# Performance work log

Measured on AMD Instinct MI355X. Metric: run time of the kernel, lower is better.

## Reference

```python
import jax, jax.numpy as jnp
import numpy as np

# pywt db4 decomposition low-pass filter (dec_lo), length 8
_DEC_LO = np.array([-0.010597401784997278, 0.032883011666982945,
                    0.030841381835986965, -0.18703481171888114,
                    -0.02798376941698385, 0.6308807679295904,
                    0.7148465705525415, 0.23037781330885523], dtype=np.float32)
FLEN = 8
LEVELS = 9            # pywt.dwt_max_level(4096, 8) == 9
# pywt computes a convolution with dec_lo == correlation with reversed dec_lo
_KERNEL = jnp.asarray(_DEC_LO[::-1].copy()).reshape(1, 1, FLEN)


def _dwt_lo(a):
    """One DWT level (approximation branch only), pywt 'symmetric' mode.
    Output length = floor((n + FLEN - 1) / 2), matching pywt.dwt."""
    pad = [(0, 0)] * (a.ndim - 1) + [(FLEN - 1, FLEN - 1)]
    p = jnp.pad(a, pad, mode='symmetric')[..., 1:]  # correlation starts at offset 1
    bflat = int(np.prod(a.shape[:-1]))
    y = jax.lax.conv_general_dilated(p.reshape(bflat, 1, -1), _KERNEL,
                                     window_strides=(2,), padding='VALID')
    return y.reshape(a.shape[:-1] + (y.shape[-1],))


def wavedec_approx(x):
    a = x
    for _ in range(LEVELS):  # fixed small level count, not a data-dim loop
        a = _dwt_lo(a)
    return a  # [..., 14]


def setup_inputs() -> dict:
    key = jax.random.key(0)
    k1, k2, k3 = jax.random.split(key, 3)
    x = jax.random.normal(k1, (32, 512, 4096), dtype=jnp.float32)
    W = jax.random.normal(k2, (14, 14), dtype=jnp.float32) * (1.0 / np.sqrt(14.0).astype(np.float32))
    b = jax.random.normal(k3, (14,), dtype=jnp.float32) * 0.01
    return {"x": x, "W": W, "b": b}


def reference(x, W, b):
    # original detaches x before the wavelet transform
    approx = wavedec_approx(jax.lax.stop_gradient(x))          # [B, S, 14]
    aug = jnp.einsum('bsf,of->bso', approx, W) + b             # Linear(14, 14)
    return jnp.concatenate([x, aug], axis=-1)                  # [B, S, 4096 + 14]
```

## Files before the change

kernel.cpp:

```cpp
#include <hip/hip_runtime.h>


#define ROWS 16384
#define N0   4096
#define OUTW 4110

__device__ __constant__ float c_dec_lo[8] = {
    -0.010597401784997278f,  0.032883011666982945f,
     0.030841381835986965f, -0.18703481171888114f,
    -0.02798376941698385f,   0.6308807679295904f,
     0.7148465705525415f,    0.23037781330885523f};

__global__ __launch_bounds__(256) void wavelet_aug_kernel(
    const float* __restrict__ x, const float* __restrict__ W,
    const float* __restrict__ b, float* __restrict__ out)
{
    __shared__ float bufA[4096];
    __shared__ float bufB[2051];

    const int row = blockIdx.x;
    const int tid = threadIdx.x;
    const float* xr  = x   + (size_t)row * N0;
    float*       outr = out + (size_t)row * OUTW;

    for (int i = tid; i < N0 / 2; i += 256) {
        float2 v = reinterpret_cast<const float2*>(xr)[i];
        reinterpret_cast<float2*>(outr)[i] = v;
        bufA[2 * i]     = v.x;
        bufA[2 * i + 1] = v.y;
    }
    __syncthreads();

    const int nin_tab[9] = {4096, 2051, 1029, 518, 262, 134, 70, 38, 22};
    float* bin  = bufA;
    float* bout = bufB;
    #pragma unroll
    for (int lev = 0; lev < 9; ++lev) {
        const int n    = nin_tab[lev];
        const int nout = (n + 7) >> 1;
        for (int i = tid; i < nout; i += 256) {
            float acc = 0.f;
            #pragma unroll
            for (int k = 0; k < 8; ++k) {
                int t = 2 * i + 1 - k;
                int idx = (t < 0) ? (-1 - t) : ((t >= n) ? (2 * n - 1 - t) : t);
                acc += bin[idx] * c_dec_lo[k];
            }
            bout[i] = acc;
        }
        __syncthreads();
        float* tmp = bin; bin = bout; bout = tmp;
    }

    if (tid < 14) {
        float acc = b[tid];
        #pragma unroll
        for (int f = 0; f < 14; ++f)
            acc += bin[f] * W[tid * 14 + f];
        outr[N0 + tid] = acc;
    }
}

extern "C" void kernel_launch(void* const* d_in, const int* in_sizes, int n_in,
                              void* d_out, int out_size, void* d_ws, size_t ws_size,
                              hipStream_t stream) {
    const float* x = (const float*)d_in[0];
    const float* W = (const float*)d_in[1];
    const float* b = (const float*)d_in[2];
    float* out = (float*)d_out;
    wavelet_aug_kernel<<<ROWS, 256, 0, stream>>>(x, W, b, out);
}
```

Baseline: 134.8 us.

## Split DWT buffers into even/odd LDS halves with vectorized interior chunks

Stores each level's coefficients deinterleaved into even and odd shared arrays, so interior outputs are computed four at a time from float4 LDS loads with no symmetric-index arithmetic. Boundary chunks keep the scalar mirrored path. The last five small levels run on one wavefront, with an lgkmcnt wait instead of block-wide barriers. This reduces LDS instruction count and barrier cost, at the price of extra code complexity and reliance on implicit wave-level synchronisation.

```diff
diff --git a/kernel.cpp b/kernel.cpp
--- a/kernel.cpp
+++ b/kernel.cpp
@@ -5,58 +5,127 @@
 #define N0   4096
 #define OUTW 4110
 
-__device__ __constant__ float c_dec_lo[8] = {
-    -0.010597401784997278f,  0.032883011666982945f,
-     0.030841381835986965f, -0.18703481171888114f,
-    -0.02798376941698385f,   0.6308807679295904f,
-     0.7148465705525415f,    0.23037781330885523f};
+#define D0 -0.010597401784997278f
+#define D1  0.032883011666982945f
+#define D2  0.030841381835986965f
+#define D3 -0.18703481171888114f
+#define D4 -0.02798376941698385f
+#define D5  0.6308807679295904f
+#define D6  0.7148465705525415f
+#define D7  0.23037781330885523f
+#define CE0 D7
+#define CE1 D5
+#define CE2 D3
+#define CE3 D1
+#define CO0 D6
+#define CO1 D4
+#define CO2 D2
+#define CO3 D0
+
+__device__ __forceinline__ void dwt_level(const float* __restrict__ ein,
+                                          const float* __restrict__ oin,
+                                          float* __restrict__ eout,
+                                          float* __restrict__ oout,
+                                          int n, int tid, int nthreads)
+{
+    const float crev[8] = {D7, D6, D5, D4, D3, D2, D1, D0};
+    const int nout = (n + 7) >> 1;
+    const int nchunks = (nout + 3) >> 2;
+    const int clast = (n - 8) >> 3;
+    for (int c = tid; c < nchunks; c += nthreads) {
+        if (c >= 1 && c <= clast) {
+            const float4 e0 = *reinterpret_cast<const float4*>(ein + 4 * c - 4);
+            const float4 e1 = *reinterpret_cast<const float4*>(ein + 4 * c);
+            const float4 o0 = *reinterpret_cast<const float4*>(oin + 4 * c - 4);
+            const float4 o1 = *reinterpret_cast<const float4*>(oin + 4 * c);
+            const float we[8] = {e0.x, e0.y, e0.z, e0.w, e1.x, e1.y, e1.z, e1.w};
+            const float wo[8] = {o0.x, o0.y, o0.z, o0.w, o1.x, o1.y, o1.z, o1.w};
+            float y[4];
+            #pragma unroll
+            for (int j = 0; j < 4; ++j) {
+                float acc =      we[j + 1] * CE0;
+                acc = fmaf(we[j + 2], CE1, acc);
+                acc = fmaf(we[j + 3], CE2, acc);
+                acc = fmaf(we[j + 4], CE3, acc);
+                acc = fmaf(wo[j + 1], CO0, acc);
+                acc = fmaf(wo[j + 2], CO1, acc);
+                acc = fmaf(wo[j + 3], CO2, acc);
+                acc = fmaf(wo[j + 4], CO3, acc);
+                y[j] = acc;
+            }
+            *reinterpret_cast<float2*>(eout + 2 * c) = make_float2(y[0], y[2]);
+            *reinterpret_cast<float2*>(oout + 2 * c) = make_float2(y[1], y[3]);
+        } else {
+            #pragma unroll
+            for (int j = 0; j < 4; ++j) {
+                const int i = 4 * c + j;
+                if (i < nout) {
+                    float acc = 0.f;
+                    #pragma unroll
+                    for (int jj = 0; jj < 8; ++jj) {
+                        int t = 2 * i - 6 + jj;
+                        int tt = (t < 0) ? (-1 - t) : ((t >= n) ? (2 * n - 1 - t) : t);
+                        float a = (tt & 1) ? oin[tt >> 1] : ein[tt >> 1];
+                        acc = fmaf(a, crev[jj], acc);
+                    }
+                    if (i & 1) oout[i >> 1] = acc;
+                    else       eout[i >> 1] = acc;
+                }
+            }
+        }
+    }
+}
+
+#define WAVE_LDS_FENCE() do {                                   \
+    asm volatile("s_waitcnt lgkmcnt(0)" ::: "memory");          \
+    __builtin_amdgcn_sched_barrier(0);                          \
+} while (0)
 
 __global__ __launch_bounds__(256) void wavelet_aug_kernel(
     const float* __restrict__ x, const float* __restrict__ W,
     const float* __restrict__ b, float* __restrict__ out)
 {
-    __shared__ float bufA[4096];
-    __shared__ float bufB[2051];
+    __shared__ __align__(16) float eA[2048];
+    __shared__ __align__(16) float oA[2048];
+    __shared__ __align__(16) float eB[1026];
+    __shared__ __align__(16) float oB[1026];
 
     const int row = blockIdx.x;
     const int tid = threadIdx.x;
-    const float* xr  = x   + (size_t)row * N0;
+    const float* xr   = x   + (size_t)row * N0;
     float*       outr = out + (size_t)row * OUTW;
 
-    for (int i = tid; i < N0 / 2; i += 256) {
-        float2 v = reinterpret_cast<const float2*>(xr)[i];
-        reinterpret_cast<float2*>(outr)[i] = v;
-        bufA[2 * i]     = v.x;
-        bufA[2 * i + 1] = v.y;
+    const float4* x4 = reinterpret_cast<const float4*>(xr);
+    float2* out2 = reinterpret_cast<float2*>(outr);
+    for (int i = tid; i < N0 / 4; i += 256) {
+        const float4 v = x4[i];
+        out2[2 * i]     = make_float2(v.x, v.y);
+        out2[2 * i + 1] = make_float2(v.z, v.w);
+        *reinterpret_cast<float2*>(eA + 2 * i) = make_float2(v.x, v.z);
+        *reinterpret_cast<float2*>(oA + 2 * i) = make_float2(v.y, v.w);
     }
     __syncthreads();
 
-    const int nin_tab[9] = {4096, 2051, 1029, 518, 262, 134, 70, 38, 22};
-    float* bin  = bufA;
-    float* bout = bufB;
-    #pragma unroll
-    for (int lev = 0; lev < 9; ++lev) {
-        const int n    = nin_tab[lev];
-        const int nout = (n + 7) >> 1;
-        for (int i = tid; i < nout; i += 256) {
-            float acc = 0.f;
-            #pragma unroll
-            for (int k = 0; k < 8; ++k) {
-                int t = 2 * i + 1 - k;
-                int idx = (t < 0) ? (-1 - t) : ((t >= n) ? (2 * n - 1 - t) : t);
-                acc += bin[idx] * c_dec_lo[k];
-            }
-            bout[i] = acc;
-        }
-        __syncthreads();
-        float* tmp = bin; bin = bout; bout = tmp;
-    }
+    dwt_level(eA, oA, eB, oB, 4096, tid, 256); __syncthreads();
+    dwt_level(eB, oB, eA, oA, 2051, tid, 256); __syncthreads();
+    dwt_level(eA, oA, eB, oB, 1029, tid, 256); __syncthreads();
+    dwt_level(eB, oB, eA, oA,  518, tid, 256); __syncthreads();
+
+    if (tid >= 64) return;
+
+    dwt_level(eA, oA, eB, oB, 262, tid, 64); WAVE_LDS_FENCE();
+    dwt_level(eB, oB, eA, oA, 134, tid, 64); WAVE_LDS_FENCE();
+    dwt_level(eA, oA, eB, oB,  70, tid, 64); WAVE_LDS_FENCE();
+    dwt_level(eB, oB, eA, oA,  38, tid, 64); WAVE_LDS_FENCE();
+    dwt_level(eA, oA, eB, oB,  22, tid, 64); WAVE_LDS_FENCE();
 
     if (tid < 14) {
         float acc = b[tid];
         #pragma unroll
-        for (int f = 0; f < 14; ++f)
-            acc += bin[f] * W[tid * 14 + f];
+        for (int f = 0; f < 14; ++f) {
+            const float a = (f & 1) ? oB[f >> 1] : eB[f >> 1];
+            acc = fmaf(a, W[tid * 14 + f], acc);
+        }
         outr[N0 + tid] = acc;
     }
 }
```

After: 203.5 us. +51.0%, slower.

## Collapse linear wavelet cascade and projection into a precomputed 14x4096 matrix

Applied to the files above, without the earlier changes.

Because the nine DWT levels and the 14x14 linear layer are all linear in x, a small pre-kernel computes the combined operator (14x4096) by propagating W rows backward through the adjoint of each symmetric-padded strided convolution. The main kernel keeps that matrix in registers and, for 16 rows per 1024-thread block, computes each output as a dot product using wave shuffles plus a shared-memory reduction, while copying x to the output. This replaces the multi-level shared-memory cascade and its per-level barriers with one streaming pass. The cost is an extra launch, a workspace buffer, and a 14x4096 matrix-vector product per row in place of the cascade's work.

```diff
diff --git a/kernel.cpp b/kernel.cpp
--- a/kernel.cpp
+++ b/kernel.cpp
@@ -5,59 +5,105 @@
 #define N0   4096
 #define OUTW 4110
 
-__device__ __constant__ float c_dec_lo[8] = {
+__device__ __constant__ float c_dlo[8] = {
     -0.010597401784997278f,  0.032883011666982945f,
      0.030841381835986965f, -0.18703481171888114f,
     -0.02798376941698385f,   0.6308807679295904f,
      0.7148465705525415f,    0.23037781330885523f};
 
-__global__ __launch_bounds__(256) void wavelet_aug_kernel(
-    const float* __restrict__ x, const float* __restrict__ W,
+__device__ __forceinline__ float adj_contrib(const float* __restrict__ g,
+                                             int t, int nout) {
+    int i0 = t >> 1;        if (i0 < 0) i0 = 0;
+    int i1 = (t + 6) >> 1;  if (i1 > nout - 1) i1 = nout - 1;
+    float acc = 0.f;
+    for (int i = i0; i <= i1; ++i)
+        acc = fmaf(g[i], c_dlo[2 * i + 1 - t], acc);
+    return acc;
+}
+
+__global__ __launch_bounds__(256) void build_cm_kernel(
+    const float* __restrict__ W, float* __restrict__ cm)
+{
+    __shared__ float A[4096];
+    __shared__ float B[2051];
+    const int o = blockIdx.x, tid = threadIdx.x;
+    if (tid < 14) B[tid] = W[o * 14 + tid];
+    __syncthreads();
+    const int ns[10] = {14, 22, 38, 70, 134, 262, 518, 1029, 2051, 4096};
+    float* g = B;
+    float* h = A;
+    for (int lev = 1; lev <= 9; ++lev) {
+        const int n = ns[lev], nout = ns[lev - 1];
+        const int s2 = 2 * (n - nout);
+        for (int s = tid; s < n; s += 256) {
+            float v = adj_contrib(g, s, nout);
+            if (s <= 5)  v += adj_contrib(g, -1 - s, nout);
+            if (s >= s2) v += adj_contrib(g, 2 * n - 1 - s, nout);
+            h[s] = v;
+        }
+        __syncthreads();
+        float* t2 = g; g = h; h = t2;
+    }
+    for (int c = tid; c < 4096; c += 256) cm[o * 4096 + c] = g[c];
+}
+
+__global__ __launch_bounds__(1024) void wavelet_aug_main(
+    const float* __restrict__ x, const float* __restrict__ cm,
     const float* __restrict__ b, float* __restrict__ out)
 {
-    __shared__ float bufA[4096];
-    __shared__ float bufB[2051];
+    __shared__ float parts[2][16][14];
+    const int tid  = threadIdx.x;
+    const int wave = tid >> 6;
+    const int lane = tid & 63;
+    const int c4   = tid << 2;
 
-    const int row = blockIdx.x;
-    const int tid = threadIdx.x;
-    const float* xr  = x   + (size_t)row * N0;
-    float*       outr = out + (size_t)row * OUTW;
+    float4 cmv[14];
+    #pragma unroll
+    for (int o = 0; o < 14; ++o)
+        cmv[o] = *reinterpret_cast<const float4*>(cm + o * N0 + c4);
+    const float bb = (tid < 14) ? b[tid] : 0.f;
 
-    for (int i = tid; i < N0 / 2; i += 256) {
-        float2 v = reinterpret_cast<const float2*>(xr)[i];
-        reinterpret_cast<float2*>(outr)[i] = v;
-        bufA[2 * i]     = v.x;
-        bufA[2 * i + 1] = v.y;
-    }
-    __syncthreads();
+    const int row0 = blockIdx.x * 16;
+    const float* xrow = x + (size_t)row0 * N0 + c4;
 
-    const int nin_tab[9] = {4096, 2051, 1029, 518, 262, 134, 70, 38, 22};
-    float* bin  = bufA;
-    float* bout = bufB;
-    #pragma unroll
-    for (int lev = 0; lev < 9; ++lev) {
-        const int n    = nin_tab[lev];
-        const int nout = (n + 7) >> 1;
-        for (int i = tid; i < nout; i += 256) {
-            float acc = 0.f;
+    float4 xa = *reinterpret_cast<const float4*>(xrow);
+    for (int r = 0; r < 16; ++r) {
+        float4 xb;
+        if (r < 15) xb = *reinterpret_cast<const float4*>(xrow + (r + 1) * N0);
+
+        float* orow = out + (size_t)(row0 + r) * OUTW + c4;
+        reinterpret_cast<float2*>(orow)[0] = make_float2(xa.x, xa.y);
+        reinterpret_cast<float2*>(orow)[1] = make_float2(xa.z, xa.w);
+
+        float acc[14];
+        #pragma unroll
+        for (int o = 0; o < 14; ++o) {
+            float v = xa.x * cmv[o].x;
+            v = fmaf(xa.y, cmv[o].y, v);
+            v = fmaf(xa.z, cmv[o].z, v);
+            v = fmaf(xa.w, cmv[o].w, v);
+            acc[o] = v;
+        }
+        #pragma unroll
+        for (int o = 0; o < 14; ++o) {
+            float v = acc[o];
+            v += __shfl_xor(v, 1);  v += __shfl_xor(v, 2);
+            v += __shfl_xor(v, 4);  v += __shfl_xor(v, 8);
+            v += __shfl_xor(v, 16); v += __shfl_xor(v, 32);
+            acc[o] = v;
+        }
+        if (lane == 0) {
             #pragma unroll
-            for (int k = 0; k < 8; ++k) {
-                int t = 2 * i + 1 - k;
-                int idx = (t < 0) ? (-1 - t) : ((t >= n) ? (2 * n - 1 - t) : t);
-                acc += bin[idx] * c_dec_lo[k];
-            }
-            bout[i] = acc;
+            for (int o = 0; o < 14; ++o) parts[r & 1][wave][o] = acc[o];
         }
         __syncthreads();
-        float* tmp = bin; bin = bout; bout = tmp;
-    }
-
-    if (tid < 14) {
-        float acc = b[tid];
-        #pragma unroll
-        for (int f = 0; f < 14; ++f)
-            acc += bin[f] * W[tid * 14 + f];
-        outr[N0 + tid] = acc;
+        if (tid < 14) {
+            float s = bb;
+            #pragma unroll
+            for (int w = 0; w < 16; ++w) s += parts[r & 1][w][tid];
+            out[(size_t)(row0 + r) * OUTW + N0 + tid] = s;
+        }
+        xa = xb;
     }
 }
 
@@ -68,5 +114,8 @@
     const float* W = (const float*)d_in[1];
     const float* b = (const float*)d_in[2];
     float* out = (float*)d_out;
-    wavelet_aug_kernel<<<ROWS, 256, 0, stream>>>(x, W, b, out);
+    float* cm  = (float*)d_ws;
+
+    build_cm_kernel<<<14, 256, 0, stream>>>(W, cm);
+    wavelet_aug_main<<<ROWS / 16, 1024, 0, stream>>>(x, cm, b, out);
 }
```

After: 287.9 us. 114% more time.
